# Performance work log

Hardware: AMD Instinct MI355X
Metric: run time of the kernel (lower is better)

## Reference

```python
import jax, jax.numpy as jnp
import numpy as np

VOCAB = 30000
K1 = 1.2
B_PARAM = 0.75


def setup_inputs() -> dict:
    key = jax.random.key(0)
    k1, k2 = jax.random.split(key)
    B, L = 2048, 512
    input_ids = jax.random.randint(k1, (B, L), 0, VOCAB, dtype=jnp.int64)
    attention_mask = jnp.ones((B, L), dtype=jnp.int64)
    W = jax.random.normal(k2, (768, VOCAB), dtype=jnp.float32) / np.sqrt(VOCAB)
    return {"input_ids": input_ids, "attention_mask": attention_mask, "W": W}


def reference(input_ids, attention_mask, W):
    B, L = input_ids.shape
    # valid tokens: attended AND 100 < id < VOCAB
    valid = (attention_mask == 1) & (input_ids > 100) & (input_ids < VOCAB)
    validf = valid.astype(jnp.float32)
    doc_len = validf.sum(-1)  # [B]

    # batched histogram (TF counts) via scatter-add; invalid entries add 0 at slot 0
    rows = jnp.broadcast_to(jnp.arange(B)[:, None], (B, L))
    toks = jnp.where(valid, input_ids, 0)
    tf = jnp.zeros((B, VOCAB), jnp.float32).at[rows, toks].add(validf)  # [B, VOCAB]

    # BM25 scoring; torch writes scores only at unique tokens -> equivalent to masking tf>0
    length_norm = jnp.maximum(1.0 + B_PARAM * (doc_len / 100.0 - 1.0), 0.5)[:, None]
    scores = jnp.where(tf > 0, tf * (K1 + 1.0) / (tf + K1 * length_norm), 0.0)

    v = scores + 1e-10
    v = v / jnp.linalg.norm(v, axis=-1, keepdims=True)  # F.normalize p=2

    out = v @ W.T  # Linear(VOCAB, 768, bias=False)
    out = out / jnp.linalg.norm(out, axis=-1, keepdims=True)
    return out
```

## Files before the change

kernel.cpp:

```cpp
#include <hip/hip_runtime.h>
#include <hip/hip_bf16.h>
#include <stdint.h>

#define B_ROWS 2048
#define SEQ 512
#define VOC 30000
#define DMODEL 768
#define K1 1.2f
#define BPAR 0.75f
#define NT 192
#define PF 8
#define TGX 235
#define TGY 12

__launch_bounds__(256)
__global__ void prep_trans(const float* __restrict__ W, __hip_bfloat16* __restrict__ Wb,
                           const int* __restrict__ ids, const int* __restrict__ mask,
                           int* __restrict__ stoks_g, float* __restrict__ wts_g,
                           int* __restrict__ n_g) {
    __shared__ ushort smem[64 * 130];
    int bid = blockIdx.x;
    int tid = threadIdx.x;

    if (bid < B_ROWS) {
        int b = bid;
        int*   stoks = (int*)smem;
        float* wts   = (float*)((char*)smem + 2048);
        int*   nvp   = (int*)((char*)smem + 4096);

        if (tid == 0) *nvp = 0;
        __syncthreads();

        for (int i = tid; i < SEQ; i += 256) {
            int id = ids[(size_t)b * SEQ + i];
            int m  = mask[(size_t)b * SEQ + i];
            if (m == 1 && id > 100 && id < VOC) {
                stoks[atomicAdd(nvp, 1)] = id;
            }
        }
        __syncthreads();
        int n = *nvp;

        for (int i = n + tid; i < SEQ; i += 256) stoks[i] = 0x7fffffff;

        for (int k = 2; k <= SEQ; k <<= 1) {
            for (int j = k >> 1; j > 0; j >>= 1) {
                __syncthreads();
                for (int i = tid; i < SEQ; i += 256) {
                    int ixj = i ^ j;
                    if (ixj > i) {
                        int a = stoks[i], c = stoks[ixj];
                        if ((a > c) == ((i & k) == 0)) { stoks[i] = c; stoks[ixj] = a; }
                    }
                }
            }
        }
        __syncthreads();

        float kln = K1 * fmaxf(1.0f + BPAR * ((float)n / 100.0f - 1.0f), 0.5f);
        for (int i = tid; i < n; i += 256) {
            int t = stoks[i];
            int lo = i; while (lo > 0 && stoks[lo - 1] == t) lo--;
            int hi = i; while (hi < n - 1 && stoks[hi + 1] == t) hi++;
            wts[i] = (K1 + 1.0f) / ((float)(hi - lo + 1) + kln);
        }
        __syncthreads();

        for (int i = tid; i < n; i += 256) {
            stoks_g[(size_t)b * SEQ + i] = stoks[i] * (DMODEL / 4);
            wts_g[(size_t)b * SEQ + i]   = wts[i];
        }
        if (tid == 0) n_g[b] = n;
    } else {
        ushort (*tile)[130] = (ushort(*)[130])smem;
        int tb = bid - B_ROWS;
        int bx = tb % TGX, by = tb / TGX;
        int tBase = bx * 128;
        int jBase = by * 64;
        int tx = tid & 63;
        int ty = tid >> 6;

#pragma unroll
        for (int jj = 0; jj < 16; jj++) {
            int j = jBase + jj * 4 + ty;
            int t = tBase + tx * 2;
            if (t < VOC) {
                float2 v = *(const float2*)(W + (size_t)j * VOC + t);
                ushort2 u;
                u.x = __bfloat16_as_ushort(__float2bfloat16(v.x));
                u.y = __bfloat16_as_ushort(__float2bfloat16(v.y));
                *(ushort2*)&tile[jj * 4 + ty][tx * 2] = u;
            }
        }
        __syncthreads();

#pragma unroll
        for (int i = 0; i < 32; i++) {
            int trow = i * 4 + ty;
            int t = tBase + trow;
            if (t < VOC) {
                ((ushort*)Wb)[(size_t)t * DMODEL + jBase + tx] = tile[tx][trow];
            }
        }
    }
}

__device__ __forceinline__ float b2f(unsigned short h) {
    union { uint32_t u; float f; } v; v.u = ((uint32_t)h) << 16; return v.f;
}

__launch_bounds__(NT, 6)
__global__ void bm25_gather(const int* __restrict__ stoks_g, const float* __restrict__ wts_g,
                            const int* __restrict__ n_g,
                            const __hip_bfloat16* __restrict__ Wb,
                            float* __restrict__ out) {
    __shared__ int   stoks[SEQ];
    __shared__ float wts[SEQ];
    __shared__ float wred[3];

    int b = blockIdx.x;
    int tid = threadIdx.x;
    int n = n_g[b];

    for (int i = tid; i < n; i += NT) {
        stoks[i] = stoks_g[(size_t)b * SEQ + i];
        wts[i]   = wts_g[(size_t)b * SEQ + i];
    }
    __syncthreads();

    const ushort4* __restrict__ Wb4 = (const ushort4*)Wb;
    float4 acc = make_float4(0.f, 0.f, 0.f, 0.f);
    int p = 0;
    for (; p + PF <= n; p += PF) {
        ushort4 r[PF];
        float   w[PF];
#pragma unroll
        for (int q = 0; q < PF; q++) {
            r[q] = Wb4[(size_t)stoks[p + q] + tid];
            w[q] = wts[p + q];
        }
#pragma unroll
        for (int q = 0; q < PF; q++) {
            acc.x = fmaf(w[q], b2f(r[q].x), acc.x);
            acc.y = fmaf(w[q], b2f(r[q].y), acc.y);
            acc.z = fmaf(w[q], b2f(r[q].z), acc.z);
            acc.w = fmaf(w[q], b2f(r[q].w), acc.w);
        }
    }
    for (; p < n; p++) {
        float w = wts[p];
        ushort4 r = Wb4[(size_t)stoks[p] + tid];
        acc.x = fmaf(w, b2f(r.x), acc.x);
        acc.y = fmaf(w, b2f(r.y), acc.y);
        acc.z = fmaf(w, b2f(r.z), acc.z);
        acc.w = fmaf(w, b2f(r.w), acc.w);
    }

    float ss = acc.x * acc.x + acc.y * acc.y + acc.z * acc.z + acc.w * acc.w;
#pragma unroll
    for (int off = 32; off > 0; off >>= 1) ss += __shfl_down(ss, off);
    if ((tid & 63) == 0) wred[tid >> 6] = ss;
    __syncthreads();
    float inv = rsqrtf(fmaxf(wred[0] + wred[1] + wred[2], 1e-30f));

    float4 o;
    o.x = acc.x * inv; o.y = acc.y * inv; o.z = acc.z * inv; o.w = acc.w * inv;
    ((float4*)(out + (size_t)b * DMODEL))[tid] = o;
}

extern "C" void kernel_launch(void* const* d_in, const int* in_sizes, int n_in,
                              void* d_out, int out_size, void* d_ws, size_t ws_size,
                              hipStream_t stream) {
    const int*   ids  = (const int*)d_in[0];
    const int*   mask = (const int*)d_in[1];
    const float* W    = (const float*)d_in[2];
    float* out = (float*)d_out;

    char* ws = (char*)d_ws;
    __hip_bfloat16* Wb = (__hip_bfloat16*)ws;
    size_t off = (size_t)VOC * DMODEL * sizeof(__hip_bfloat16);
    int*   stoks_g = (int*)(ws + off);        off += (size_t)B_ROWS * SEQ * 4;
    float* wts_g   = (float*)(ws + off);      off += (size_t)B_ROWS * SEQ * 4;
    int*   n_g     = (int*)(ws + off);

    prep_trans<<<B_ROWS + TGX * TGY, 256, 0, stream>>>(W, Wb, ids, mask,
                                                       stoks_g, wts_g, n_g);

    bm25_gather<<<B_ROWS, NT, 0, stream>>>(stoks_g, wts_g, n_g, Wb, out);
}
```

Before: 142.8 us.

## Split gather block into two token halves with 16-byte loads and LDS reduction

The gather kernel now has 96 lanes per half, each loading 16 bytes (8 bf16) per token row instead of 8 bytes. The two halves of the block take alternating tokens, and their partial sums are combined through shared memory. The goal is wider memory transactions and two tokens in flight per block. The cost is an extra shared-memory reduction, two more barriers, and more accumulator registers, with the prefetch depth reduced to 4.

Result: slower. 183.7 us (+28.6%).

```diff
diff --git a/kernel.cpp b/kernel.cpp
--- a/kernel.cpp
+++ b/kernel.cpp
@@ -9,7 +9,7 @@
 #define K1 1.2f
 #define BPAR 0.75f
 #define NT 192
-#define PF 8
+#define PF 4
 #define TGX 235
 #define TGY 12
 
@@ -67,7 +67,7 @@
         __syncthreads();
 
         for (int i = tid; i < n; i += 256) {
-            stoks_g[(size_t)b * SEQ + i] = stoks[i] * (DMODEL / 4);
+            stoks_g[(size_t)b * SEQ + i] = stoks[i] * (DMODEL / 8);
             wts_g[(size_t)b * SEQ + i]   = wts[i];
         }
         if (tid == 0) n_g[b] = n;
@@ -105,8 +105,11 @@
     }
 }
 
-__device__ __forceinline__ float b2f(unsigned short h) {
-    union { uint32_t u; float f; } v; v.u = ((uint32_t)h) << 16; return v.f;
+__device__ __forceinline__ float bl(uint32_t d) {
+    union { uint32_t u; float f; } v; v.u = d << 16; return v.f;
+}
+__device__ __forceinline__ float bh(uint32_t d) {
+    union { uint32_t u; float f; } v; v.u = d & 0xffff0000u; return v.f;
 }
 
 __launch_bounds__(NT, 6)
@@ -116,10 +119,13 @@
                             float* __restrict__ out) {
     __shared__ int   stoks[SEQ];
     __shared__ float wts[SEQ];
+    __shared__ float accred[DMODEL];
     __shared__ float wred[3];
 
     int b = blockIdx.x;
     int tid = threadIdx.x;
+    int lane = tid % 96;
+    int half = tid / 96;
     int n = n_g[b];
 
     for (int i = tid; i < n; i += NT) {
@@ -128,35 +134,59 @@
     }
     __syncthreads();
 
-    const ushort4* __restrict__ Wb4 = (const ushort4*)Wb;
-    float4 acc = make_float4(0.f, 0.f, 0.f, 0.f);
+    const char* __restrict__ Wbase = (const char*)Wb;
+    float acc[8] = {0.f, 0.f, 0.f, 0.f, 0.f, 0.f, 0.f, 0.f};
     int p = 0;
-    for (; p + PF <= n; p += PF) {
-        ushort4 r[PF];
-        float   w[PF];
+    int npair = n & ~1;
+
+    for (; p + 2 * PF <= npair; p += 2 * PF) {
+        uint4 r[PF]; float w[PF];
 #pragma unroll
         for (int q = 0; q < PF; q++) {
-            r[q] = Wb4[(size_t)stoks[p + q] + tid];
-            w[q] = wts[p + q];
+            int pp = p + q * 2 + half;
+            r[q] = *(const uint4*)(Wbase + ((size_t)stoks[pp] + lane) * 16);
+            w[q] = wts[pp];
         }
 #pragma unroll
         for (int q = 0; q < PF; q++) {
-            acc.x = fmaf(w[q], b2f(r[q].x), acc.x);
-            acc.y = fmaf(w[q], b2f(r[q].y), acc.y);
-            acc.z = fmaf(w[q], b2f(r[q].z), acc.z);
-            acc.w = fmaf(w[q], b2f(r[q].w), acc.w);
-        }
-    }
-    for (; p < n; p++) {
-        float w = wts[p];
-        ushort4 r = Wb4[(size_t)stoks[p] + tid];
-        acc.x = fmaf(w, b2f(r.x), acc.x);
-        acc.y = fmaf(w, b2f(r.y), acc.y);
-        acc.z = fmaf(w, b2f(r.z), acc.z);
-        acc.w = fmaf(w, b2f(r.w), acc.w);
-    }
-
-    float ss = acc.x * acc.x + acc.y * acc.y + acc.z * acc.z + acc.w * acc.w;
+            acc[0] = fmaf(w[q], bl(r[q].x), acc[0]);
+            acc[1] = fmaf(w[q], bh(r[q].x), acc[1]);
+            acc[2] = fmaf(w[q], bl(r[q].y), acc[2]);
+            acc[3] = fmaf(w[q], bh(r[q].y), acc[3]);
+            acc[4] = fmaf(w[q], bl(r[q].z), acc[4]);
+            acc[5] = fmaf(w[q], bh(r[q].z), acc[5]);
+            acc[6] = fmaf(w[q], bl(r[q].w), acc[6]);
+            acc[7] = fmaf(w[q], bh(r[q].w), acc[7]);
+        }
+    }
+    if (half == 0) {
+        for (; p < n; p++) {
+            float w = wts[p];
+            uint4 r = *(const uint4*)(Wbase + ((size_t)stoks[p] + lane) * 16);
+            acc[0] = fmaf(w, bl(r.x), acc[0]);
+            acc[1] = fmaf(w, bh(r.x), acc[1]);
+            acc[2] = fmaf(w, bl(r.y), acc[2]);
+            acc[3] = fmaf(w, bh(r.y), acc[3]);
+            acc[4] = fmaf(w, bl(r.z), acc[4]);
+            acc[5] = fmaf(w, bh(r.z), acc[5]);
+            acc[6] = fmaf(w, bl(r.w), acc[6]);
+            acc[7] = fmaf(w, bh(r.w), acc[7]);
+        }
+    }
+
+    if (half == 1) {
+#pragma unroll
+        for (int d = 0; d < 8; d++) accred[lane * 8 + d] = acc[d];
+    }
+    __syncthreads();
+    if (half == 0) {
+#pragma unroll
+        for (int d = 0; d < 8; d++) accred[lane * 8 + d] += acc[d];
+    }
+    __syncthreads();
+
+    float4 a4 = ((const float4*)accred)[tid];
+    float ss = a4.x * a4.x + a4.y * a4.y + a4.z * a4.z + a4.w * a4.w;
 #pragma unroll
     for (int off = 32; off > 0; off >>= 1) ss += __shfl_down(ss, off);
     if ((tid & 63) == 0) wred[tid >> 6] = ss;
@@ -164,7 +194,7 @@
     float inv = rsqrtf(fmaxf(wred[0] + wred[1] + wred[2], 1e-30f));
 
     float4 o;
-    o.x = acc.x * inv; o.y = acc.y * inv; o.z = acc.z * inv; o.w = acc.w * inv;
+    o.x = a4.x * inv; o.y = a4.y * inv; o.z = a4.z * inv; o.w = a4.w * inv;
     ((float4*)(out + (size_t)b * DMODEL))[tid] = o;
 }
 
```
